# Kernel optimization log

Measured on AMD Instinct MI355X. Metric: run time of the kernel, lower is better.

Reference implementation:

```python
import jax, jax.numpy as jnp
import numpy as np

BASE_TEMP = 0.07
CLASS_TEMPS = jnp.array([0.08, 0.05, 0.10], dtype=jnp.float32)  # idx 0,1,2
EPS = 1e-08


def setup_inputs() -> dict:
    key = jax.random.key(0)
    k1, k2 = jax.random.split(key)
    B, D = 8192, 128
    embeddings = jax.random.normal(k1, (B, D), dtype=jnp.float32)
    labels = jax.random.randint(k2, (B,), 0, 3, dtype=jnp.int64)
    return {"embeddings": embeddings, "labels": labels}


def reference(embeddings, labels):
    B = embeddings.shape[0]
    # per-row temperature from the row's class label
    temps = CLASS_TEMPS[labels]  # [B]
    sim = jnp.matmul(embeddings, embeddings.T)  # [B, B]
    logits = sim / temps[:, None]
    # subtract detached row max (stability, gradient-stopped as in .detach())
    logits = logits - jax.lax.stop_gradient(jnp.max(logits, axis=1, keepdims=True))
    # denominator includes the self term (original sums exp over all j)
    log_prob = logits - jnp.log(jnp.sum(jnp.exp(logits), axis=1, keepdims=True) + EPS)
    # positives: same label, excluding self
    pos_mask = (labels[:, None] == labels[None, :]).astype(jnp.float32)
    pos_mask = pos_mask * (1.0 - jnp.eye(B, dtype=jnp.float32))
    pos_count = jnp.sum(pos_mask, axis=1)  # [B]
    valid = pos_count > 0
    loss_i = -(BASE_TEMP / temps) * jnp.sum(pos_mask * log_prob, axis=1) / (pos_count + EPS)
    n_valid = jnp.sum(valid.astype(jnp.float32))
    total = jnp.sum(jnp.where(valid, loss_i, 0.0))
    return jnp.where(n_valid > 0, total / jnp.maximum(n_valid, 1.0), 0.0)
```

## Files before the change

### kernel.cpp

```cpp
#include <hip/hip_runtime.h>
#include <hip/hip_bf16.h>


#define B_ROWS 8192
#define D_DIM 128
#define BASE_TEMP 0.07f
#define LOG2E 1.4426950408889634f
#define LN2 0.6931471805599453f
#define FIX_SCALE 1048576.0f

typedef __bf16 bf16x8 __attribute__((ext_vector_type(8)));
typedef __bf16 bf16x4 __attribute__((ext_vector_type(4)));
typedef float floatx16 __attribute__((ext_vector_type(16)));

__device__ __forceinline__ float class_invtemp(int lbl) {
    return (lbl == 0) ? 12.5f : ((lbl == 1) ? 20.0f : 10.0f);
}

__device__ __forceinline__ unsigned long long fix64(float v) {
    return (unsigned long long)(long long)llrintf(v * FIX_SCALE);
}

__global__ __launch_bounds__(256) void k0_prep(
        const float* __restrict__ E, const int* __restrict__ labels,
        __bf16* __restrict__ Ebf, float* __restrict__ nrm,
        unsigned long long* __restrict__ Sfix ,
        unsigned long long* __restrict__ cntfix ) {
    const int blk = blockIdx.x;
    const int tid = threadIdx.x;
    const int row0 = blk * 32;

    __shared__ float sh[3][128];
    __shared__ int scnt[3];
    if (tid < 3) scnt[tid] = 0;

    const float4* src = reinterpret_cast<const float4*>(E + (size_t)row0 * D_DIM);
    #pragma unroll
    for (int p = 0; p < 4; ++p) {
        int idx = p * 256 + tid;
        float4 v = src[idx];
        int r = idx >> 5, k4 = idx & 31;
        int R = row0 + r;
        int T = R >> 5;
        int l = (R & 31) + ((k4 >> 1) & 1) * 32;
        int c = k4 >> 2;
        size_t dst = (size_t)T * 4096 + c * 512 + l * 8 + (k4 & 1) * 4;
        bf16x4 o = { (__bf16)v.x, (__bf16)v.y, (__bf16)v.z, (__bf16)v.w };
        *reinterpret_cast<bf16x4*>(Ebf + dst) = o;
    }

    {
        int r = tid >> 3, g = tid & 7;
        const float4* er = reinterpret_cast<const float4*>(
            E + (size_t)(row0 + r) * D_DIM + g * 16);
        float s = 0.f;
        #pragma unroll
        for (int q = 0; q < 4; ++q) {
            float4 v = er[q];
            s += v.x * v.x + v.y * v.y + v.z * v.z + v.w * v.w;
        }
        s += __shfl_xor(s, 1); s += __shfl_xor(s, 2); s += __shfl_xor(s, 4);
        if (g == 0) nrm[row0 + r] = s;
    }

    const int d = tid & 127, half = tid >> 7;
    float s0 = 0.f, s1 = 0.f, s2 = 0.f;
    #pragma unroll 4
    for (int r2 = 0; r2 < 16; ++r2) {
        int r = row0 + half * 16 + r2;
        float v = E[(size_t)r * D_DIM + d];
        int l = labels[r];
        s0 += (l == 0) ? v : 0.f;
        s1 += (l == 1) ? v : 0.f;
        s2 += (l == 2) ? v : 0.f;
    }
    if (half == 1) { sh[0][d] = s0; sh[1][d] = s1; sh[2][d] = s2; }
    __syncthreads();
    if (half == 0) {
        atomicAdd(&Sfix[d],       fix64(s0 + sh[0][d]));
        atomicAdd(&Sfix[128 + d], fix64(s1 + sh[1][d]));
        atomicAdd(&Sfix[256 + d], fix64(s2 + sh[2][d]));
    }
    if (tid < 32) atomicAdd(&scnt[labels[row0 + tid]], 1);
    __syncthreads();
    if (tid < 3) atomicAdd(&cntfix[tid], (unsigned long long)scnt[tid]);
}

__global__ __launch_bounds__(256, 3) void k2_stats(
        const __bf16* __restrict__ Ebf, const int* __restrict__ labels,
        const float* __restrict__ nrm, float* __restrict__ part,
        int nsplit, int jrange) {
    const int lane = threadIdx.x & 63;
    const int wave = threadIdx.x >> 6;
    const int split = blockIdx.y;
    const int j0 = split * jrange;
    const int col = lane & 31;
    const int icol = blockIdx.x * 128 + wave * 32 + col;

    const float bscale = class_invtemp(labels[icol]) * LOG2E;
    const float m = bscale * nrm[icol];

    const int iT = blockIdx.x * 4 + wave;
    const __bf16* bbase = Ebf + (size_t)iT * 4096 + lane * 8;
    bf16x8 Bf[8];
    #pragma unroll
    for (int c = 0; c < 8; ++c) {
        bf16x8 raw = *reinterpret_cast<const bf16x8*>(bbase + c * 512);
        bf16x8 sc;
        #pragma unroll
        for (int e = 0; e < 8; ++e) sc[e] = (__bf16)((float)raw[e] * bscale);
        Bf[c] = sc;
    }

    const __bf16* abase = Ebf + ((size_t)(j0 >> 5)) * 4096 + lane * 8;
    bf16x8 A0[8], A1[8];
    #pragma unroll
    for (int c = 0; c < 8; ++c)
        A0[c] = *reinterpret_cast<const bf16x8*>(abase + c * 512);

    float Z0 = 0.f, Z1 = 0.f;
    const int nsteps = jrange >> 5;

    auto k2_step = [&](const bf16x8* Ab, float& Zc) {
        floatx16 a0, a1;
        #pragma unroll
        for (int r = 0; r < 16; ++r) { a0[r] = -m; a1[r] = 0.f; }
        a0 = __builtin_amdgcn_mfma_f32_32x32x16_bf16(Ab[0], Bf[0], a0, 0, 0, 0);
        a1 = __builtin_amdgcn_mfma_f32_32x32x16_bf16(Ab[4], Bf[4], a1, 0, 0, 0);
        a0 = __builtin_amdgcn_mfma_f32_32x32x16_bf16(Ab[1], Bf[1], a0, 0, 0, 0);
        a1 = __builtin_amdgcn_mfma_f32_32x32x16_bf16(Ab[5], Bf[5], a1, 0, 0, 0);
        a0 = __builtin_amdgcn_mfma_f32_32x32x16_bf16(Ab[2], Bf[2], a0, 0, 0, 0);
        a1 = __builtin_amdgcn_mfma_f32_32x32x16_bf16(Ab[6], Bf[6], a1, 0, 0, 0);
        a0 = __builtin_amdgcn_mfma_f32_32x32x16_bf16(Ab[3], Bf[3], a0, 0, 0, 0);
        a1 = __builtin_amdgcn_mfma_f32_32x32x16_bf16(Ab[7], Bf[7], a1, 0, 0, 0);
        float z[16];
        #pragma unroll
        for (int r = 0; r < 16; ++r)
            z[r] = __builtin_amdgcn_exp2f(a0[r] + a1[r]);
        float t0 = (z[0] + z[1]) + (z[2] + z[3]);
        float t1 = (z[4] + z[5]) + (z[6] + z[7]);
        float t2 = (z[8] + z[9]) + (z[10] + z[11]);
        float t3 = (z[12] + z[13]) + (z[14] + z[15]);
        Zc += (t0 + t1) + (t2 + t3);
    };

    for (int s = 0; s < nsteps; s += 2) {
        {
            const __bf16* ap = abase + (size_t)(s + 1) * 4096;
            #pragma unroll
            for (int c = 0; c < 8; ++c)
                A1[c] = *reinterpret_cast<const bf16x8*>(ap + c * 512);
            k2_step(A0, Z0);
        }
        {
            if (s + 2 < nsteps) {
                const __bf16* ap = abase + (size_t)(s + 2) * 4096;
                #pragma unroll
                for (int c = 0; c < 8; ++c)
                    A0[c] = *reinterpret_cast<const bf16x8*>(ap + c * 512);
            }
            k2_step(A1, Z1);
        }
    }

    float Zt = Z0 + Z1;
    Zt += __shfl_xor(Zt, 32);
    if (lane < 32)
        part[(size_t)split * B_ROWS + icol] = Zt;
}

__global__ __launch_bounds__(128) void k3_rowloss(
        const float* __restrict__ E, const int* __restrict__ labels,
        const unsigned long long* __restrict__ Sfix,
        const unsigned long long* __restrict__ cntfix,
        const float* __restrict__ nrm, const float* __restrict__ part,
        int nsplit, unsigned long long* __restrict__ lossfix,
        unsigned long long* __restrict__ validfix) {
    __shared__ float sS[3][128];
    const int tid = threadIdx.x;
    #pragma unroll
    for (int c = 0; c < 3; ++c)
        sS[c][tid] = (float)(long long)Sfix[c * 128 + tid] * (1.0f / FIX_SCALE);
    __syncthreads();

    const int i = blockIdx.x * 128 + tid;
    const int lab = labels[i];
    const float invt = class_invtemp(lab);

    const float4* er = reinterpret_cast<const float4*>(E + (size_t)i * D_DIM);
    const float4* sr = reinterpret_cast<const float4*>(&sS[lab][0]);
    float dotS = 0.f;
    #pragma unroll
    for (int k4 = 0; k4 < 32; ++k4) {
        float4 v = er[k4];
        float4 s = sr[k4];
        dotS += v.x * s.x + v.y * s.y + v.z * s.z + v.w * s.w;
    }
    const float nr = nrm[i];

    float Zt = 0.f;
    for (int sp = 0; sp < nsplit; ++sp)
        Zt += part[(size_t)sp * B_ROWS + i];

    const float C = (float)(long long)cntfix[lab] - 1.0f;
    const float lse = invt * nr + LN2 * __builtin_amdgcn_logf(Zt);
    const float P_nat = invt * (dotS - nr);
    float loss = -(BASE_TEMP * invt) * (P_nat - C * lse) / (C + 1e-8f);
    int valid = (C > 0.f) ? 1 : 0;
    loss = (C > 0.f) ? loss : 0.f;

    #pragma unroll
    for (int off = 32; off; off >>= 1) {
        loss += __shfl_down(loss, off);
        valid += __shfl_down(valid, off);
    }
    __shared__ float rl[2];
    __shared__ int rv[2];
    if ((tid & 63) == 0) { rl[tid >> 6] = loss; rv[tid >> 6] = valid; }
    __syncthreads();
    if (tid == 0) {
        atomicAdd(lossfix, fix64(rl[0] + rl[1]));
        atomicAdd(validfix, (unsigned long long)(rv[0] + rv[1]));
    }
}

__global__ void k4_final(const unsigned long long* __restrict__ lossfix,
                         const unsigned long long* __restrict__ validfix,
                         float* __restrict__ out) {
    if (threadIdx.x == 0) {
        double T = (double)(long long)lossfix[0] * (1.0 / (double)FIX_SCALE);
        float N = (float)(long long)validfix[0];
        out[0] = (N > 0.f) ? (float)(T / (double)fmaxf(N, 1.f)) : 0.f;
    }
}

extern "C" void kernel_launch(void* const* d_in, const int* in_sizes, int n_in,
                              void* d_out, int out_size, void* d_ws, size_t ws_size,
                              hipStream_t stream) {
    const float* E = (const float*)d_in[0];
    const int* labels = (const int*)d_in[1];
    float* out = (float*)d_out;
    char* ws = (char*)d_ws;

    const size_t OFF_EBF = 0;
    const size_t OFF_ATOM = (size_t)2 << 20;
    const size_t OFF_NRM = OFF_ATOM + 4096;
    const size_t OFF_PART = OFF_NRM + (size_t)B_ROWS * 4;

    int nsplit = 8;
    if (ws_size >= OFF_PART + (size_t)32 * B_ROWS * 4) nsplit = 32;
    else if (ws_size >= OFF_PART + (size_t)16 * B_ROWS * 4) nsplit = 16;
    const int jrange = B_ROWS / nsplit;

    __bf16* Ebf = (__bf16*)(ws + OFF_EBF);
    unsigned long long* Sfix = (unsigned long long*)(ws + OFF_ATOM);
    unsigned long long* cntfix = Sfix + 384;
    unsigned long long* lossfix = Sfix + 388;
    unsigned long long* validfix = Sfix + 389;
    float* nrm = (float*)(ws + OFF_NRM);
    float* part = (float*)(ws + OFF_PART);

    hipMemsetAsync(ws + OFF_ATOM, 0, 4096, stream);
    k0_prep<<<256, 256, 0, stream>>>(E, labels, Ebf, nrm, Sfix, cntfix);
    k2_stats<<<dim3(64, nsplit), 256, 0, stream>>>(Ebf, labels, nrm, part, nsplit, jrange);
    k3_rowloss<<<64, 128, 0, stream>>>(E, labels, Sfix, cntfix, nrm, part,
                                       nsplit, lossfix, validfix);
    k4_final<<<1, 64, 0, stream>>>(lossfix, validfix, out);
}
```

Before: 50.82 us.

## Fuse final reduction into row-loss kernel, replace memset, restructure MFMA chain

Replaces hipMemsetAsync with a tiny zeroing kernel and folds the final-division kernel into k3 through a last-block-done atomic counter, cutting launch overhead. k3 now uses 8 threads per row across 256 blocks for more parallelism in the dot product and partial-sum gather. k0 computes norms from the already-loaded values instead of reloading. k2 switches from two interleaved MFMA accumulators to a single dependent chain with per-register Z accumulators, which serialises MFMA latency but saves the per-step horizontal adds.

```diff
diff --git a/kernel.cpp b/kernel.cpp
--- a/kernel.cpp
+++ b/kernel.cpp
@@ -12,20 +12,25 @@
 typedef __bf16 bf16x8 __attribute__((ext_vector_type(8)));
 typedef __bf16 bf16x4 __attribute__((ext_vector_type(4)));
 typedef float floatx16 __attribute__((ext_vector_type(16)));
+typedef unsigned long long u64;
 
 __device__ __forceinline__ float class_invtemp(int lbl) {
     return (lbl == 0) ? 12.5f : ((lbl == 1) ? 20.0f : 10.0f);
 }
 
-__device__ __forceinline__ unsigned long long fix64(float v) {
-    return (unsigned long long)(long long)llrintf(v * FIX_SCALE);
+__device__ __forceinline__ u64 fix64(float v) {
+    return (u64)(long long)llrintf(v * FIX_SCALE);
+}
+
+__global__ __launch_bounds__(256) void kz_zero(u64* __restrict__ a) {
+    a[threadIdx.x] = 0ull;
+    a[256 + threadIdx.x] = 0ull;
 }
 
 __global__ __launch_bounds__(256) void k0_prep(
         const float* __restrict__ E, const int* __restrict__ labels,
         __bf16* __restrict__ Ebf, float* __restrict__ nrm,
-        unsigned long long* __restrict__ Sfix ,
-        unsigned long long* __restrict__ cntfix ) {
+        u64* __restrict__ Sfix , u64* __restrict__ cntfix ) {
     const int blk = blockIdx.x;
     const int tid = threadIdx.x;
     const int row0 = blk * 32;
@@ -47,20 +52,10 @@
         size_t dst = (size_t)T * 4096 + c * 512 + l * 8 + (k4 & 1) * 4;
         bf16x4 o = { (__bf16)v.x, (__bf16)v.y, (__bf16)v.z, (__bf16)v.w };
         *reinterpret_cast<bf16x4*>(Ebf + dst) = o;
-    }
-
-    {
-        int r = tid >> 3, g = tid & 7;
-        const float4* er = reinterpret_cast<const float4*>(
-            E + (size_t)(row0 + r) * D_DIM + g * 16);
-        float s = 0.f;
-        #pragma unroll
-        for (int q = 0; q < 4; ++q) {
-            float4 v = er[q];
-            s += v.x * v.x + v.y * v.y + v.z * v.z + v.w * v.w;
-        }
-        s += __shfl_xor(s, 1); s += __shfl_xor(s, 2); s += __shfl_xor(s, 4);
-        if (g == 0) nrm[row0 + r] = s;
+        float s = v.x * v.x + v.y * v.y + v.z * v.z + v.w * v.w;
+        s += __shfl_xor(s, 1);  s += __shfl_xor(s, 2);  s += __shfl_xor(s, 4);
+        s += __shfl_xor(s, 8);  s += __shfl_xor(s, 16);
+        if ((tid & 31) == 0) nrm[R] = s;
     }
 
     const int d = tid & 127, half = tid >> 7;
@@ -83,7 +78,7 @@
     }
     if (tid < 32) atomicAdd(&scnt[labels[row0 + tid]], 1);
     __syncthreads();
-    if (tid < 3) atomicAdd(&cntfix[tid], (unsigned long long)scnt[tid]);
+    if (tid < 3) atomicAdd(&cntfix[tid], (u64)scnt[tid]);
 }
 
 __global__ __launch_bounds__(256, 3) void k2_stats(
@@ -98,7 +93,7 @@
     const int icol = blockIdx.x * 128 + wave * 32 + col;
 
     const float bscale = class_invtemp(labels[icol]) * LOG2E;
-    const float m = bscale * nrm[icol];
+    const float negm = -bscale * nrm[icol];
 
     const int iT = blockIdx.x * 4 + wave;
     const __bf16* bbase = Ebf + (size_t)iT * 4096 + lane * 8;
@@ -118,30 +113,21 @@
     for (int c = 0; c < 8; ++c)
         A0[c] = *reinterpret_cast<const bf16x8*>(abase + c * 512);
 
-    float Z0 = 0.f, Z1 = 0.f;
+    float Zacc[16];
+    #pragma unroll
+    for (int r = 0; r < 16; ++r) Zacc[r] = 0.f;
     const int nsteps = jrange >> 5;
 
-    auto k2_step = [&](const bf16x8* Ab, float& Zc) {
-        floatx16 a0, a1;
-        #pragma unroll
-        for (int r = 0; r < 16; ++r) { a0[r] = -m; a1[r] = 0.f; }
-        a0 = __builtin_amdgcn_mfma_f32_32x32x16_bf16(Ab[0], Bf[0], a0, 0, 0, 0);
-        a1 = __builtin_amdgcn_mfma_f32_32x32x16_bf16(Ab[4], Bf[4], a1, 0, 0, 0);
-        a0 = __builtin_amdgcn_mfma_f32_32x32x16_bf16(Ab[1], Bf[1], a0, 0, 0, 0);
-        a1 = __builtin_amdgcn_mfma_f32_32x32x16_bf16(Ab[5], Bf[5], a1, 0, 0, 0);
-        a0 = __builtin_amdgcn_mfma_f32_32x32x16_bf16(Ab[2], Bf[2], a0, 0, 0, 0);
-        a1 = __builtin_amdgcn_mfma_f32_32x32x16_bf16(Ab[6], Bf[6], a1, 0, 0, 0);
-        a0 = __builtin_amdgcn_mfma_f32_32x32x16_bf16(Ab[3], Bf[3], a0, 0, 0, 0);
-        a1 = __builtin_amdgcn_mfma_f32_32x32x16_bf16(Ab[7], Bf[7], a1, 0, 0, 0);
-        float z[16];
+    auto k2_step = [&](const bf16x8* Ab) {
+        floatx16 acc;
+        #pragma unroll
+        for (int r = 0; r < 16; ++r) acc[r] = negm;
+        #pragma unroll
+        for (int c = 0; c < 8; ++c)
+            acc = __builtin_amdgcn_mfma_f32_32x32x16_bf16(Ab[c], Bf[c], acc, 0, 0, 0);
         #pragma unroll
         for (int r = 0; r < 16; ++r)
-            z[r] = __builtin_amdgcn_exp2f(a0[r] + a1[r]);
-        float t0 = (z[0] + z[1]) + (z[2] + z[3]);
-        float t1 = (z[4] + z[5]) + (z[6] + z[7]);
-        float t2 = (z[8] + z[9]) + (z[10] + z[11]);
-        float t3 = (z[12] + z[13]) + (z[14] + z[15]);
-        Zc += (t0 + t1) + (t2 + t3);
+            Zacc[r] += __builtin_amdgcn_exp2f(acc[r]);
     };
 
     for (int s = 0; s < nsteps; s += 2) {
@@ -150,7 +136,7 @@
             #pragma unroll
             for (int c = 0; c < 8; ++c)
                 A1[c] = *reinterpret_cast<const bf16x8*>(ap + c * 512);
-            k2_step(A0, Z0);
+            k2_step(A0);
         }
         {
             if (s + 2 < nsteps) {
@@ -159,78 +145,93 @@
                 for (int c = 0; c < 8; ++c)
                     A0[c] = *reinterpret_cast<const bf16x8*>(ap + c * 512);
             }
-            k2_step(A1, Z1);
-        }
-    }
-
-    float Zt = Z0 + Z1;
+            k2_step(A1);
+        }
+    }
+
+    float t0 = (Zacc[0] + Zacc[1]) + (Zacc[2] + Zacc[3]);
+    float t1 = (Zacc[4] + Zacc[5]) + (Zacc[6] + Zacc[7]);
+    float t2 = (Zacc[8] + Zacc[9]) + (Zacc[10] + Zacc[11]);
+    float t3 = (Zacc[12] + Zacc[13]) + (Zacc[14] + Zacc[15]);
+    float Zt = (t0 + t1) + (t2 + t3);
     Zt += __shfl_xor(Zt, 32);
     if (lane < 32)
         part[(size_t)split * B_ROWS + icol] = Zt;
 }
 
-__global__ __launch_bounds__(128) void k3_rowloss(
+__global__ __launch_bounds__(256) void k3_rowloss(
         const float* __restrict__ E, const int* __restrict__ labels,
-        const unsigned long long* __restrict__ Sfix,
-        const unsigned long long* __restrict__ cntfix,
+        const u64* __restrict__ Sfix, const u64* __restrict__ cntfix,
         const float* __restrict__ nrm, const float* __restrict__ part,
-        int nsplit, unsigned long long* __restrict__ lossfix,
-        unsigned long long* __restrict__ validfix) {
-    __shared__ float sS[3][128];
+        int nsplit, u64* __restrict__ lossfix, u64* __restrict__ validfix,
+        unsigned int* __restrict__ done, float* __restrict__ out) {
+    __shared__ float sS[384];
     const int tid = threadIdx.x;
-    #pragma unroll
-    for (int c = 0; c < 3; ++c)
-        sS[c][tid] = (float)(long long)Sfix[c * 128 + tid] * (1.0f / FIX_SCALE);
-    __syncthreads();
-
-    const int i = blockIdx.x * 128 + tid;
+    if (tid < 128) {
+        sS[tid]       = (float)(long long)Sfix[tid]       * (1.0f / FIX_SCALE);
+        sS[128 + tid] = (float)(long long)Sfix[128 + tid] * (1.0f / FIX_SCALE);
+        sS[256 + tid] = (float)(long long)Sfix[256 + tid] * (1.0f / FIX_SCALE);
+    }
+    __syncthreads();
+
+    const int r = tid >> 3, g = tid & 7;
+    const int i = blockIdx.x * 32 + r;
     const int lab = labels[i];
     const float invt = class_invtemp(lab);
 
     const float4* er = reinterpret_cast<const float4*>(E + (size_t)i * D_DIM);
-    const float4* sr = reinterpret_cast<const float4*>(&sS[lab][0]);
+    const float4* sr = reinterpret_cast<const float4*>(&sS[lab * 128]);
     float dotS = 0.f;
     #pragma unroll
-    for (int k4 = 0; k4 < 32; ++k4) {
-        float4 v = er[k4];
-        float4 s = sr[k4];
+    for (int q = 0; q < 4; ++q) {
+        float4 v = er[g * 4 + q];
+        float4 s = sr[g * 4 + q];
         dotS += v.x * s.x + v.y * s.y + v.z * s.z + v.w * s.w;
     }
-    const float nr = nrm[i];
-
-    float Zt = 0.f;
-    for (int sp = 0; sp < nsplit; ++sp)
-        Zt += part[(size_t)sp * B_ROWS + i];
-
-    const float C = (float)(long long)cntfix[lab] - 1.0f;
-    const float lse = invt * nr + LN2 * __builtin_amdgcn_logf(Zt);
-    const float P_nat = invt * (dotS - nr);
-    float loss = -(BASE_TEMP * invt) * (P_nat - C * lse) / (C + 1e-8f);
-    int valid = (C > 0.f) ? 1 : 0;
-    loss = (C > 0.f) ? loss : 0.f;
-
-    #pragma unroll
-    for (int off = 32; off; off >>= 1) {
-        loss += __shfl_down(loss, off);
-        valid += __shfl_down(valid, off);
-    }
-    __shared__ float rl[2];
-    __shared__ int rv[2];
+    float Zp = 0.f;
+    for (int p = g; p < nsplit; p += 8)
+        Zp += part[(size_t)p * B_ROWS + i];
+
+    #pragma unroll
+    for (int off = 1; off < 8; off <<= 1) {
+        dotS += __shfl_xor(dotS, off);
+        Zp   += __shfl_xor(Zp, off);
+    }
+
+    float loss = 0.f;
+    int valid = 0;
+    if (g == 0) {
+        const float nr = nrm[i];
+        const float C = (float)(long long)cntfix[lab] - 1.0f;
+        const float lse = invt * nr + LN2 * __builtin_amdgcn_logf(Zp);
+        const float P_nat = invt * (dotS - nr);
+        if (C > 0.f) {
+            loss = -(BASE_TEMP * invt) * (P_nat - C * lse) / (C + 1e-8f);
+            valid = 1;
+        }
+    }
+    loss  += __shfl_down(loss, 8);   valid += __shfl_down(valid, 8);
+    loss  += __shfl_down(loss, 16);  valid += __shfl_down(valid, 16);
+    loss  += __shfl_down(loss, 32);  valid += __shfl_down(valid, 32);
+
+    __shared__ float rl[4];
+    __shared__ int rv[4];
     if ((tid & 63) == 0) { rl[tid >> 6] = loss; rv[tid >> 6] = valid; }
     __syncthreads();
     if (tid == 0) {
-        atomicAdd(lossfix, fix64(rl[0] + rl[1]));
-        atomicAdd(validfix, (unsigned long long)(rv[0] + rv[1]));
-    }
-}
-
-__global__ void k4_final(const unsigned long long* __restrict__ lossfix,
-                         const unsigned long long* __restrict__ validfix,
-                         float* __restrict__ out) {
-    if (threadIdx.x == 0) {
-        double T = (double)(long long)lossfix[0] * (1.0 / (double)FIX_SCALE);
-        float N = (float)(long long)validfix[0];
-        out[0] = (N > 0.f) ? (float)(T / (double)fmaxf(N, 1.f)) : 0.f;
+        float bt = (rl[0] + rl[1]) + (rl[2] + rl[3]);
+        int bv = (rv[0] + rv[1]) + (rv[2] + rv[3]);
+        atomicAdd(lossfix, fix64(bt));
+        atomicAdd(validfix, (u64)bv);
+        __threadfence();
+        unsigned int t = atomicAdd(done, 1u);
+        if (t == gridDim.x - 1) {
+            u64 L = atomicAdd(lossfix, 0ull);
+            u64 V = atomicAdd(validfix, 0ull);
+            double T = (double)(long long)L * (1.0 / (double)FIX_SCALE);
+            double N = (double)(long long)V;
+            out[0] = (N > 0.0) ? (float)(T / fmax(N, 1.0)) : 0.f;
+        }
     }
 }
 
@@ -253,17 +254,17 @@
     const int jrange = B_ROWS / nsplit;
 
     __bf16* Ebf = (__bf16*)(ws + OFF_EBF);
-    unsigned long long* Sfix = (unsigned long long*)(ws + OFF_ATOM);
-    unsigned long long* cntfix = Sfix + 384;
-    unsigned long long* lossfix = Sfix + 388;
-    unsigned long long* validfix = Sfix + 389;
+    u64* Sfix = (u64*)(ws + OFF_ATOM);
+    u64* cntfix = Sfix + 384;
+    u64* lossfix = Sfix + 388;
+    u64* validfix = Sfix + 389;
+    unsigned int* done = (unsigned int*)(Sfix + 390);
     float* nrm = (float*)(ws + OFF_NRM);
     float* part = (float*)(ws + OFF_PART);
 
-    hipMemsetAsync(ws + OFF_ATOM, 0, 4096, stream);
+    kz_zero<<<1, 256, 0, stream>>>(Sfix);
     k0_prep<<<256, 256, 0, stream>>>(E, labels, Ebf, nrm, Sfix, cntfix);
     k2_stats<<<dim3(64, nsplit), 256, 0, stream>>>(Ebf, labels, nrm, part, nsplit, jrange);
-    k3_rowloss<<<64, 128, 0, stream>>>(E, labels, Sfix, cntfix, nrm, part,
-                                       nsplit, lossfix, validfix);
-    k4_final<<<1, 64, 0, stream>>>(lossfix, validfix, out);
-}
+    k3_rowloss<<<256, 256, 0, stream>>>(E, labels, Sfix, cntfix, nrm, part,
+                                        nsplit, lossfix, validfix, done, out);
+}
```

New measurement: 55.57 us. +9.3%, slower.
